# Optimization experiments

Measured on AMD Instinct MI355X. Metric: run time of the kernel, lower is better.

## Reference

```python
import jax, jax.numpy as jnp
import numpy as np


def setup_inputs() -> dict:
    key = jax.random.key(0)
    k1, k2 = jax.random.split(key)
    B, C, H, W = 2, 512, 128, 256
    refimg_fea = jax.random.normal(k1, (B, C, H, W), dtype=jnp.float32)
    targetimg_fea = jax.random.normal(k2, (B, C, H, W), dtype=jnp.float32)
    return {
        "refimg_fea": refimg_fea,
        "targetimg_fea": targetimg_fea,
        "num_groups": 8,
        "maxdisp": 48,
    }


def reference(refimg_fea, targetimg_fea, num_groups, maxdisp):
    # Group-wise correlation cost volume.
    # Torch version: left-pad target by (maxdisp-1), unfold width-maxdisp windows,
    # multiply with ref, sum over per-group channels, then flip the disparity axis.
    # Equivalent direct form: volume[b,g,d,h,w] = sum_c ref[b,g,c,h,w] * tgt[b,g,c,h,w-d]
    # (zero where w-d < 0), for d in [0, maxdisp).
    B, C, H, W = refimg_fea.shape
    G = num_groups
    Cg = C // G
    ref = refimg_fea.reshape(B, G, Cg, H, W)
    tgt = targetimg_fea.reshape(B, G, Cg, H, W)
    # zero-pad target on the left of the width axis
    padded = jnp.pad(tgt, ((0, 0), (0, 0), (0, 0), (0, 0), (maxdisp - 1, 0)))
    slices = []
    for d in range(maxdisp):  # small fixed loop over disparities (static slices)
        start = maxdisp - 1 - d
        tgt_d = padded[..., start:start + W]  # target shifted right by d
        slices.append(jnp.einsum('bgchw,bgchw->bghw', ref, tgt_d))
    volume = jnp.stack(slices, axis=2)  # [B, G, maxdisp, H, W]
    return volume
```

## Files before the change

kernel.cpp:

```cpp
#include <hip/hip_runtime.h>

#define NBG 16
#define HH 128
#define WW 256
#define CGR 64
#define ND 48
#define TPB 256
#define PITCH 40
#define OPITCH 132

typedef __attribute__((ext_vector_type(8))) short short8v;
typedef __attribute__((ext_vector_type(4))) float float4v;

__device__ __forceinline__ short f2bf(float x) {
    unsigned u = __builtin_bit_cast(unsigned, x);
    u += 0x7fffu + ((u >> 16) & 1u);
    return (short)(u >> 16);
}

__global__ __launch_bounds__(TPB, 4)
void gwc_mfma(const float* __restrict__ ref, const float* __restrict__ tgt,
              float* __restrict__ out) {
    __shared__ __align__(16) short refT[128][PITCH];
    __shared__ __align__(16) short tgtT[176][PITCH];
    __shared__ __align__(16) float outb[ND][OPITCH];

    const int tid  = threadIdx.x;
    const int lane = tid & 63;
    const int wv   = tid >> 6;
    const int fr   = lane & 15;
    const int fhi  = lane >> 4;

    const int blk  = blockIdx.x;
    const int half = blk & 1;
    const int h    = (blk >> 1) & (HH - 1);
    const int bg   = blk >> 8;
    const int W0   = half * 128;

    const size_t cstride = (size_t)HH * WW;
    const float* refbase = ref + ((size_t)bg * CGR * HH + h) * WW;
    const float* tgtbase = tgt + ((size_t)bg * CGR * HH + h) * WW;

    float4v acc[2][4];
    #pragma unroll
    for (int j = 0; j < 2; ++j)
        #pragma unroll
        for (int i = 0; i < 4; ++i)
            acc[j][i] = (float4v){0.f, 0.f, 0.f, 0.f};

    for (int ch = 0; ch < 2; ++ch) {
        if (ch) __syncthreads();
        const int c0 = ch * 32;
        #pragma unroll
        for (int rr = 0; rr < 2; ++rr) {
            const int row = tid + rr * 256;
            if (row < 304) {
                const bool isref = row < 128;
                const int  r  = isref ? row : row - 128;
                const int  wg = isref ? (W0 + r) : (W0 - 48 + r);
                short* dst = isref ? &refT[r][0] : &tgtT[r][0];
                if (wg >= 0) {
                    const float* p = (isref ? refbase : tgtbase) + (size_t)c0 * cstride + wg;
                    float v[32];
                    #pragma unroll
                    for (int cc = 0; cc < 32; ++cc) v[cc] = p[(size_t)cc * cstride];
                    #pragma unroll
                    for (int gq = 0; gq < 8; ++gq)
                        *(short4*)(dst + 4 * gq) =
                            make_short4(f2bf(v[4*gq]), f2bf(v[4*gq+1]),
                                        f2bf(v[4*gq+2]), f2bf(v[4*gq+3]));
                } else {
                    #pragma unroll
                    for (int gq = 0; gq < 8; ++gq)
                        *(short4*)(dst + 4 * gq) = make_short4(0, 0, 0, 0);
                }
            }
        }
        __syncthreads();
        const short8v bfr0 = *(const short8v*)&refT[16 * wv + fr][8 * fhi];
        const short8v bfr1 = *(const short8v*)&refT[16 * (wv + 4) + fr][8 * fhi];
        #pragma unroll
        for (int j = 0; j < 2; ++j) {
            #pragma unroll
            for (int i = 0; i < 4; ++i) {
                const int mt = wv + 4 * j + i;
                const short8v afr = *(const short8v*)&tgtT[16 * mt + fr][8 * fhi];
                acc[j][i] = __builtin_amdgcn_mfma_f32_16x16x32_bf16(
                    afr, (j ? bfr1 : bfr0), acc[j][i], 0, 0, 0);
            }
        }
    }

    #pragma unroll
    for (int j = 0; j < 2; ++j) {
        const int wl = 16 * (wv + 4 * j) + fr;
        #pragma unroll
        for (int i = 0; i < 4; ++i)
            #pragma unroll
            for (int rg = 0; rg < 4; ++rg) {
                const int d = 48 - 16 * i + fr - 4 * fhi - rg;
                if ((unsigned)d < (unsigned)ND)
                    outb[d][wl] = acc[j][i][rg];
            }
    }
    __syncthreads();
    for (int s = tid; s < ND * 32; s += TPB) {
        const int dd = s >> 5;
        const int wq = s & 31;
        const float4 v = *(const float4*)&outb[dd][4 * wq];
        *(float4*)(out + ((size_t)(bg * ND + dd) * HH + h) * WW + W0 + 4 * wq) = v;
    }
}

extern "C" void kernel_launch(void* const* d_in, const int* in_sizes, int n_in,
                              void* d_out, int out_size, void* d_ws, size_t ws_size,
                              hipStream_t stream) {
    const float* ref = (const float*)d_in[0];
    const float* tgt = (const float*)d_in[1];
    float* out = (float*)d_out;
    const int grid = NBG * HH * 2;
    gwc_mfma<<<dim3(grid), dim3(TPB), 0, stream>>>(ref, tgt, out);
}
```

Before: 76.52 us.

## Retile group correlation to two rows per block with swizzled LDS and coalesced loads

Each block now covers two full image rows of one batch-group with 512 threads, instead of a half row. Loads change from strided per-channel scalar gathers to float4 segments along the width axis. Values are converted to bf16 and stored into a XOR-swizzled, channel-interleaved shared-memory layout that the MFMA fragments then read, with 16-channel chunks processed over four iterations. The output staging buffer reuses the same shared memory, blocks are reordered for locality, and the redundant target halo loads from the half-row split are gone. The cost is more synchronisation, half the lanes sitting idle with zero fragments in each MFMA, and larger LDS use that may limit occupancy.

```diff
diff --git a/kernel.cpp b/kernel.cpp
--- a/kernel.cpp
+++ b/kernel.cpp
@@ -1,13 +1,12 @@
 #include <hip/hip_runtime.h>
 
-#define NBG 16
 #define HH 128
 #define WW 256
-#define CGR 64
 #define ND 48
-#define TPB 256
-#define PITCH 40
-#define OPITCH 132
+#define TPB 512
+#define CCH 16
+#define RP 18
+#define OP 264
 
 typedef __attribute__((ext_vector_type(8))) short short8v;
 typedef __attribute__((ext_vector_type(4))) float float4v;
@@ -18,97 +17,137 @@
     return (short)(u >> 16);
 }
 
+__device__ __forceinline__ short8v ldfrag(const short* rowp, int S, int k0h) {
+    union { int i[4]; short8v v; } u;
+    #pragma unroll
+    for (int m = 0; m < 4; ++m) u.i[m] = *(const int*)(rowp + 2 * ((k0h + m) ^ S));
+    return u.v;
+}
+
 __global__ __launch_bounds__(TPB, 4)
 void gwc_mfma(const float* __restrict__ ref, const float* __restrict__ tgt,
               float* __restrict__ out) {
-    __shared__ __align__(16) short refT[128][PITCH];
-    __shared__ __align__(16) short tgtT[176][PITCH];
-    __shared__ __align__(16) float outb[ND][OPITCH];
+    __shared__ __align__(16) char smem[50688];
+    short* sref = (short*)smem;
+    short* stgt = (short*)(smem + 18432);
+    float* outb = (float*)smem;
 
     const int tid  = threadIdx.x;
     const int lane = tid & 63;
     const int wv   = tid >> 6;
     const int fr   = lane & 15;
     const int fhi  = lane >> 4;
+    const int hw   = wv & 1;
+    const int ntg  = wv >> 1;
 
-    const int blk  = blockIdx.x;
-    const int half = blk & 1;
-    const int h    = (blk >> 1) & (HH - 1);
-    const int bg   = blk >> 8;
-    const int W0   = half * 128;
+    const int blk = ((blockIdx.x & 7) << 7) | (blockIdx.x >> 3);
+    const int bg  = blk >> 6;
+    const int h0  = (blk & 63) << 1;
 
-    const size_t cstride = (size_t)HH * WW;
-    const float* refbase = ref + ((size_t)bg * CGR * HH + h) * WW;
-    const float* tgtbase = tgt + ((size_t)bg * CGR * HH + h) * WW;
+    for (int i = tid; i < 864; i += TPB) ((int*)stgt)[i] = 0;
 
-    float4v acc[2][4];
+    const int sc_ = tid >> 5;
+    const int sh  = (tid >> 4) & 1;
+    const int seg = tid & 15;
+    const float* rptr0 = ref + ((size_t)(bg * 64 + sc_) * HH + (h0 + sh)) * WW + 16 * seg;
+    const float* tptr0 = tgt + ((size_t)(bg * 64 + sc_) * HH + (h0 + sh)) * WW + 16 * seg;
+    const size_t cstep = (size_t)CCH * HH * WW;
+    const int scr = 2 * ((sc_ >> 1) ^ (seg & 7) ^ (sh << 2)) + (sc_ & 1);
+    const int sct = 2 * ((sc_ >> 1) ^ ((seg + 3) & 7) ^ (sh << 2)) + (sc_ & 1);
+
+    float4v acc[4][4];
     #pragma unroll
-    for (int j = 0; j < 2; ++j)
+    for (int n = 0; n < 4; ++n)
         #pragma unroll
-        for (int i = 0; i < 4; ++i)
-            acc[j][i] = (float4v){0.f, 0.f, 0.f, 0.f};
+        for (int t = 0; t < 4; ++t) acc[n][t] = (float4v){0.f, 0.f, 0.f, 0.f};
 
-    for (int ch = 0; ch < 2; ++ch) {
-        if (ch) __syncthreads();
-        const int c0 = ch * 32;
+    for (int ch = 0; ch < 4; ++ch) {
+        float4 g0, g1, g2, g3, t0, t1, t2, t3;
+        {
+            const float* rp = rptr0 + ch * cstep;
+            const float* tp = tptr0 + ch * cstep;
+            g0 = *(const float4*)(rp + 0);  g1 = *(const float4*)(rp + 4);
+            g2 = *(const float4*)(rp + 8);  g3 = *(const float4*)(rp + 12);
+            t0 = *(const float4*)(tp + 0);  t1 = *(const float4*)(tp + 4);
+            t2 = *(const float4*)(tp + 8);  t3 = *(const float4*)(tp + 12);
+        }
+        __syncthreads();
+#define WRT(J, V)                                                                  \
+        {                                                                          \
+            const int wbase = 16 * seg + 4 * J;                                    \
+            sref[((wbase + 0) * 2 + sh) * RP + scr] = f2bf(V.x);                   \
+            sref[((wbase + 1) * 2 + sh) * RP + scr] = f2bf(V.y);                   \
+            sref[((wbase + 2) * 2 + sh) * RP + scr] = f2bf(V.z);                   \
+            sref[((wbase + 3) * 2 + sh) * RP + scr] = f2bf(V.w);                   \
+        }
+#define WTT(J, V)                                                                  \
+        {                                                                          \
+            const int rbase = 16 * seg + 4 * J + 48;                               \
+            stgt[((rbase + 0) * 2 + sh) * RP + sct] = f2bf(V.x);                   \
+            stgt[((rbase + 1) * 2 + sh) * RP + sct] = f2bf(V.y);                   \
+            stgt[((rbase + 2) * 2 + sh) * RP + sct] = f2bf(V.z);                   \
+            stgt[((rbase + 3) * 2 + sh) * RP + sct] = f2bf(V.w);                   \
+        }
+        WRT(0, g0) WRT(1, g1) WRT(2, g2) WRT(3, g3)
+        WTT(0, t0) WTT(1, t1) WTT(2, t2) WTT(3, t3)
+#undef WRT
+#undef WTT
+        __syncthreads();
+        short8v bf[4], af[7];
+        if (fhi < 2) {
+            const int k0h = 4 * fhi;
+            #pragma unroll
+            for (int n = 0; n < 4; ++n) {
+                const int NT = 4 * ntg + n;
+                bf[n] = ldfrag(&sref[((16 * NT + fr) * 2 + hw) * RP],
+                               (NT & 7) ^ (hw << 2), k0h);
+            }
+            #pragma unroll
+            for (int m = 0; m < 7; ++m) {
+                const int MT = 4 * ntg + m;
+                af[m] = ldfrag(&stgt[((16 * MT + fr) * 2 + hw) * RP],
+                               (MT & 7) ^ (hw << 2), k0h);
+            }
+        } else {
+            #pragma unroll
+            for (int n = 0; n < 4; ++n) bf[n] = (short8v){0,0,0,0,0,0,0,0};
+            #pragma unroll
+            for (int m = 0; m < 7; ++m) af[m] = (short8v){0,0,0,0,0,0,0,0};
+        }
         #pragma unroll
-        for (int rr = 0; rr < 2; ++rr) {
-            const int row = tid + rr * 256;
-            if (row < 304) {
-                const bool isref = row < 128;
-                const int  r  = isref ? row : row - 128;
-                const int  wg = isref ? (W0 + r) : (W0 - 48 + r);
-                short* dst = isref ? &refT[r][0] : &tgtT[r][0];
-                if (wg >= 0) {
-                    const float* p = (isref ? refbase : tgtbase) + (size_t)c0 * cstride + wg;
-                    float v[32];
+        for (int n = 0; n < 4; ++n)
+            #pragma unroll
+            for (int t = 0; t < 4; ++t)
+                acc[n][t] = __builtin_amdgcn_mfma_f32_16x16x32_bf16(
+                                af[n + t], bf[n], acc[n][t], 0, 0, 0);
+    }
+
+    __syncthreads();
+    #pragma unroll
+    for (int ph = 0; ph < 2; ++ph) {
+        if (hw == ph) {
+            #pragma unroll
+            for (int n = 0; n < 4; ++n) {
+                const int wl = 16 * (4 * ntg + n) + fr;
+                #pragma unroll
+                for (int t = 0; t < 4; ++t)
                     #pragma unroll
-                    for (int cc = 0; cc < 32; ++cc) v[cc] = p[(size_t)cc * cstride];
-                    #pragma unroll
-                    for (int gq = 0; gq < 8; ++gq)
-                        *(short4*)(dst + 4 * gq) =
-                            make_short4(f2bf(v[4*gq]), f2bf(v[4*gq+1]),
-                                        f2bf(v[4*gq+2]), f2bf(v[4*gq+3]));
-                } else {
-                    #pragma unroll
-                    for (int gq = 0; gq < 8; ++gq)
-                        *(short4*)(dst + 4 * gq) = make_short4(0, 0, 0, 0);
-                }
+                    for (int rg = 0; rg < 4; ++rg) {
+                        const int d = 48 - 16 * t + fr - 4 * fhi - rg;
+                        if ((unsigned)d < (unsigned)ND) outb[d * OP + wl] = acc[n][t][rg];
+                    }
             }
         }
         __syncthreads();
-        const short8v bfr0 = *(const short8v*)&refT[16 * wv + fr][8 * fhi];
-        const short8v bfr1 = *(const short8v*)&refT[16 * (wv + 4) + fr][8 * fhi];
         #pragma unroll
-        for (int j = 0; j < 2; ++j) {
-            #pragma unroll
-            for (int i = 0; i < 4; ++i) {
-                const int mt = wv + 4 * j + i;
-                const short8v afr = *(const short8v*)&tgtT[16 * mt + fr][8 * fhi];
-                acc[j][i] = __builtin_amdgcn_mfma_f32_16x16x32_bf16(
-                    afr, (j ? bfr1 : bfr0), acc[j][i], 0, 0, 0);
-            }
+        for (int j = 0; j < 6; ++j) {
+            const int idx = tid + 512 * j;
+            const int dd  = idx >> 6;
+            const int wq  = idx & 63;
+            *(float4*)(out + ((size_t)(bg * ND + dd) * HH + h0 + ph) * WW + 4 * wq) =
+                *(const float4*)&outb[dd * OP + 4 * wq];
         }
-    }
-
-    #pragma unroll
-    for (int j = 0; j < 2; ++j) {
-        const int wl = 16 * (wv + 4 * j) + fr;
-        #pragma unroll
-        for (int i = 0; i < 4; ++i)
-            #pragma unroll
-            for (int rg = 0; rg < 4; ++rg) {
-                const int d = 48 - 16 * i + fr - 4 * fhi - rg;
-                if ((unsigned)d < (unsigned)ND)
-                    outb[d][wl] = acc[j][i][rg];
-            }
-    }
-    __syncthreads();
-    for (int s = tid; s < ND * 32; s += TPB) {
-        const int dd = s >> 5;
-        const int wq = s & 31;
-        const float4 v = *(const float4*)&outb[dd][4 * wq];
-        *(float4*)(out + ((size_t)(bg * ND + dd) * HH + h) * WW + W0 + 4 * wq) = v;
+        if (ph == 0) __syncthreads();
     }
 }
 
@@ -118,6 +157,5 @@
     const float* ref = (const float*)d_in[0];
     const float* tgt = (const float*)d_in[1];
     float* out = (float*)d_out;
-    const int grid = NBG * HH * 2;
-    gwc_mfma<<<dim3(grid), dim3(TPB), 0, stream>>>(ref, tgt, out);
+    gwc_mfma<<<dim3(16 * 64), dim3(TPB), 0, stream>>>(ref, tgt, out);
 }
```

Measured after the change: 127.2 us. +66.2%, slower.
